# Kernel tuning notes

Measured on AMD Instinct MI355X. Metric: run time of the kernel, lower is better.

The kernel has to match this reference:

```python
import jax, jax.numpy as jnp
import numpy as np

N_NODES = 50000
N_EDGES = 800000
D_IN = 768
D_H = 256
N_CLASSES = 4
N_LAYERS = 3
N_GRAPHS = 64
LN_EPS = 1e-5


def setup_inputs() -> dict:
    key = jax.random.key(0)
    ks = jax.random.split(key, 12)
    x = jax.random.normal(ks[0], (N_NODES, D_IN), dtype=jnp.float32)
    edge_index = jax.random.randint(ks[1], (2, N_EDGES), 0, N_NODES)
    batch = jnp.sort(jax.random.randint(ks[2], (N_NODES,), 0, N_GRAPHS))
    s_in = 1.0 / np.sqrt(D_IN)
    s_h = 1.0 / np.sqrt(D_H)
    W_in = jax.random.normal(ks[3], (D_IN, D_H), jnp.float32) * s_in
    b_in = jnp.zeros((D_H,), jnp.float32)
    convW = jax.random.normal(ks[4], (N_LAYERS, D_H, D_H), jnp.float32) * s_h
    convB = jnp.zeros((N_LAYERS, D_H), jnp.float32)
    lnG = jnp.ones((N_LAYERS, D_H), jnp.float32)
    lnB = jnp.zeros((N_LAYERS, D_H), jnp.float32)
    clsW1 = jax.random.normal(ks[5], (D_H, D_H), jnp.float32) * s_h
    clsB1 = jnp.zeros((D_H,), jnp.float32)
    clsW2 = jax.random.normal(ks[6], (D_H, N_CLASSES), jnp.float32) * s_h
    clsB2 = jnp.zeros((N_CLASSES,), jnp.float32)
    return {"x": x, "edge_index": edge_index, "batch": batch,
            "W_in": W_in, "b_in": b_in, "convW": convW, "convB": convB,
            "lnG": lnG, "lnB": lnB, "clsW1": clsW1, "clsB1": clsB1,
            "clsW2": clsW2, "clsB2": clsB2}


def _layer_norm(h, g, b):
    mu = jnp.mean(h, axis=-1, keepdims=True)
    var = jnp.mean(jnp.square(h - mu), axis=-1, keepdims=True)
    return (h - mu) * jax.lax.rsqrt(var + LN_EPS) * g + b


def reference(x, edge_index, batch, W_in, b_in, convW, convB, lnG, lnB,
              clsW1, clsB1, clsW2, clsB2):
    N = x.shape[0]
    loops = jnp.arange(N)
    src = jnp.concatenate([edge_index[0], loops])  # self-loops (PyG GCNConv default)
    dst = jnp.concatenate([edge_index[1], loops])
    deg = jax.ops.segment_sum(jnp.ones_like(src, dtype=x.dtype), dst, num_segments=N)
    dinv = jax.lax.rsqrt(deg)  # deg >= 1 due to self-loops
    norm = dinv[src] * dinv[dst]  # symmetric GCN normalization per edge

    h = x @ W_in + b_in  # input projection -> [N, D_H]
    for i in range(N_LAYERS):
        m = h @ convW[i]  # transform then propagate
        h_new = jax.ops.segment_sum(m[src] * norm[:, None], dst, num_segments=N) + convB[i]
        h = jax.nn.relu(h_new + h)  # residual (shapes match), then ReLU
        h = _layer_norm(h, lnG[i], lnB[i])
        # dropout: identity (inference mode)

    g = jax.ops.segment_max(h, batch, num_segments=N_GRAPHS)  # global_max_pool
    z = jax.nn.relu(g @ clsW1 + clsB1)
    return z @ clsW2 + clsB2  # [N_GRAPHS, N_CLASSES]
```

## Files before the change

kernel.cpp:

```cpp
#include <hip/hip_runtime.h>
#include <hip/hip_bf16.h>
#include <math.h>

#define NNODES 50000
#define NEDGES 800000
#define DIN 768
#define DH 256
#define NCLS 4
#define NGRAPHS 64
#define SCAN_BLOCKS 196
#define PBLK 782
#define PS 24

typedef __bf16 bf16x8 __attribute__((ext_vector_type(8)));
typedef float f32x4 __attribute__((ext_vector_type(4)));

static __device__ __forceinline__ float bf2f(unsigned short u) {
    union { unsigned u32; float f; } v; v.u32 = ((unsigned)u) << 16; return v.f;
}
static __device__ __forceinline__ unsigned short f2bf(float f) {
    union { float f; unsigned u; } v; v.f = f;
    unsigned r = (v.u + 0x7fffu + ((v.u >> 16) & 1u)) >> 16;
    return (unsigned short)r;
}
static __device__ __forceinline__ void unpack8(uint4 u, float* f) {
    f[0] = bf2f((unsigned short)(u.x & 0xffff)); f[1] = bf2f((unsigned short)(u.x >> 16));
    f[2] = bf2f((unsigned short)(u.y & 0xffff)); f[3] = bf2f((unsigned short)(u.y >> 16));
    f[4] = bf2f((unsigned short)(u.z & 0xffff)); f[5] = bf2f((unsigned short)(u.z >> 16));
    f[6] = bf2f((unsigned short)(u.w & 0xffff)); f[7] = bf2f((unsigned short)(u.w >> 16));
}
static __device__ __forceinline__ void acc8(uint4 u, float* f) {
    f[0] += bf2f((unsigned short)(u.x & 0xffff)); f[1] += bf2f((unsigned short)(u.x >> 16));
    f[2] += bf2f((unsigned short)(u.y & 0xffff)); f[3] += bf2f((unsigned short)(u.y >> 16));
    f[4] += bf2f((unsigned short)(u.z & 0xffff)); f[5] += bf2f((unsigned short)(u.z >> 16));
    f[6] += bf2f((unsigned short)(u.w & 0xffff)); f[7] += bf2f((unsigned short)(u.w >> 16));
}
static __device__ __forceinline__ uint4 pack8f(float4 f0, float4 f1) {
    uint4 u;
    u.x = (unsigned)f2bf(f0.x) | ((unsigned)f2bf(f0.y) << 16);
    u.y = (unsigned)f2bf(f0.z) | ((unsigned)f2bf(f0.w) << 16);
    u.z = (unsigned)f2bf(f1.x) | ((unsigned)f2bf(f1.y) << 16);
    u.w = (unsigned)f2bf(f1.z) | ((unsigned)f2bf(f1.w) << 16);
    return u;
}
static __device__ __forceinline__ void gload_lds16(const void* g, void* l) {
    __builtin_amdgcn_global_load_lds((const __attribute__((address_space(1))) void*)g,
                                     (__attribute__((address_space(3))) void*)l, 16, 0, 0);
}

__global__ void detect_dtype(const unsigned short* __restrict__ x, int* __restrict__ flag) {
    __shared__ int cnt_s;
    if (threadIdx.x == 0) cnt_s = 0;
    __syncthreads();
    int c = 0;
    for (int i = 0; i < 16; ++i) {
        float v = bf2f(x[threadIdx.x * 16 + i]);
        if (!(fabsf(v) < 1e10f)) c++;
    }
    atomicAdd(&cnt_s, c);
    __syncthreads();
    if (threadIdx.x == 0) flag[0] = (cnt_s > 32) ? 1 : 0;
}

static __device__ __forceinline__ unsigned short cload(const void* src, int i, int fp32) {
    return fp32 ? f2bf(((const float*)src)[i]) : ((const unsigned short*)src)[i];
}

__global__ void canon_small(const void* b_in, const void* convB, const void* lnG,
                            const void* lnB, const void* W1, const void* W2,
                            const void* b1, const void* b2,
                            unsigned short* __restrict__ dst, const int* __restrict__ flag) {
    int i = blockIdx.x * 256 + threadIdx.x;
    if (i >= 69380) return;
    const int fp32 = flag[0];
    int j = i;
    if (j < 256)  { dst[i] = cload(b_in, j, fp32); return; }  j -= 256;
    if (j < 768)  { dst[i] = cload(convB, j, fp32); return; } j -= 768;
    if (j < 768)  { dst[i] = cload(lnG, j, fp32); return; }   j -= 768;
    if (j < 768)  { dst[i] = cload(lnB, j, fp32); return; }   j -= 768;
    if (j < 65536){ dst[i] = cload(W1, j, fp32); return; }    j -= 65536;
    if (j < 1024) { dst[i] = cload(W2, j, fp32); return; }    j -= 1024;
    if (j < 256)  { dst[i] = cload(b1, j, fp32); return; }    j -= 256;
    dst[i] = cload(b2, j, fp32);
}

__global__ void transpose_win(const void* __restrict__ src, unsigned short* __restrict__ dst,
                              const int* __restrict__ flag) {
    int idx = blockIdx.x * 256 + threadIdx.x;
    if (idx < DIN * DH) {
        int r = idx / DH, c = idx % DH;
        dst[(size_t)c * DIN + r] = cload(src, idx, flag[0]);
    }
}
__global__ void transpose_convw(const void* __restrict__ src, unsigned short* __restrict__ dst,
                                const int* __restrict__ flag) {
    int idx = blockIdx.x * 256 + threadIdx.x;
    if (idx < 3 * DH * DH) {
        int l = idx >> 16, rc = idx & 65535;
        int r = rc >> 8, c = rc & 255;
        dst[(l << 16) + c * DH + r] = cload(src, idx, flag[0]);
    }
}

__global__ __launch_bounds__(256) void pack_a(
    const void* __restrict__ x, const int* __restrict__ flag,
    uint4* __restrict__ out)
{
    const int c = blockIdx.x * 256 + threadIdx.x;
    const int blk = c / 6144;
    const int rem = c - blk * 6144;
    const int s = rem >> 8;
    const int q = rem & 255;
    const int r = q >> 2, p = q & 3;
    const int l = p ^ ((r >> 1) & 3);
    const int row = blk * 64 + r;
    const int k0 = s * 32 + l * 8;
    uint4 v = make_uint4(0u, 0u, 0u, 0u);
    if (row < NNODES) {
        if (flag[0]) {
            const float* xf = (const float*)x + (size_t)row * DIN + k0;
            float4 f0 = *(const float4*)xf;
            float4 f1 = *(const float4*)(xf + 4);
            v = pack8f(f0, f1);
        } else {
            v = *(const uint4*)((const unsigned short*)x + (size_t)row * DIN + k0);
        }
    }
    out[c] = v;
}

__global__ void fill_sentinel(float* out, int n) {
    int i = blockIdx.x * 256 + threadIdx.x;
    if (i < n) out[i] = 1000.0f;
}

__global__ void count_edges(const int* __restrict__ ei, int* __restrict__ cnt) {
    int e = blockIdx.x * 256 + threadIdx.x;
    if (e < NEDGES) atomicAdd(&cnt[ei[NEDGES + e]], 1);
}

__global__ void scan_local(const int* __restrict__ cnt, int* __restrict__ rowptr,
                           int* __restrict__ bsum) {
    __shared__ int tmp[256];
    int i = blockIdx.x * 256 + threadIdx.x;
    int v = (i < NNODES) ? cnt[i] : 0;
    tmp[threadIdx.x] = v;
    __syncthreads();
    for (int off = 1; off < 256; off <<= 1) {
        int a = (threadIdx.x >= off) ? tmp[threadIdx.x - off] : 0;
        __syncthreads();
        tmp[threadIdx.x] += a;
        __syncthreads();
    }
    if (i < NNODES) rowptr[i] = tmp[threadIdx.x] - v;
    if (threadIdx.x == 255) bsum[blockIdx.x] = tmp[255];
}
__global__ void scan_bsum(const int* __restrict__ bsum, int* __restrict__ boff) {
    __shared__ int tmp[256];
    int t = threadIdx.x;
    int v = (t < SCAN_BLOCKS) ? bsum[t] : 0;
    tmp[t] = v;
    __syncthreads();
    for (int off = 1; off < 256; off <<= 1) {
        int a = (t >= off) ? tmp[t - off] : 0;
        __syncthreads();
        tmp[t] += a;
        __syncthreads();
    }
    if (t < SCAN_BLOCKS) boff[t] = tmp[t] - v;
}
__global__ void scan_finish(int* __restrict__ rowptr, const int* __restrict__ boff,
                            const int* __restrict__ cnt, float* __restrict__ dinv) {
    int i = blockIdx.x * 256 + threadIdx.x;
    if (i < NNODES) {
        rowptr[i] += boff[blockIdx.x];
        dinv[i] = rsqrtf((float)(1 + cnt[i]));
    }
    if (i == 0) rowptr[NNODES] = NEDGES;
}

__global__ void fill_csr(const int* __restrict__ ei, const int* __restrict__ rowptr,
                         int* __restrict__ cursor, int* __restrict__ csrc) {
    int e = blockIdx.x * 256 + threadIdx.x;
    if (e < NEDGES) {
        int s = ei[e];
        int d = ei[NEDGES + e];
        int pos = rowptr[d] + atomicAdd(&cursor[d], 1);
        csrc[pos] = s;
    }
}

template<int WF>
__global__ __launch_bounds__(256, WF == 1 ? 3 : 4) void gemm_core(
    const void* __restrict__ Araw, const int* __restrict__ dflag,
    const unsigned short* __restrict__ Bt, const unsigned short* __restrict__ bias,
    const float* __restrict__ prescale, unsigned short* __restrict__ C, int M, int K)
{
    __shared__ __align__(16) char As[2][WF == 1 ? 8192 : 4096];
    __shared__ __align__(16) char Bs[2][16384];

    const int af32 = (WF == 1) ? dflag[0] : 0;
    const int m0 = blockIdx.x * 64;
    const int t = threadIdx.x, wave = t >> 6, lane = t & 63;
    const int quad = lane >> 4, l16 = lane & 15;

    const char* bsrc[4];
#pragma unroll
    for (int li = 0; li < 4; ++li) {
        int c = wave * 256 + li * 64 + lane;
        int r = c >> 2, p = c & 3;
        int l = p ^ ((r >> 1) & 3);
        bsrc[li] = (const char*)Bt + ((size_t)r * K + l * 8) * 2;
    }
    const char* asrc[2];
    if (WF == 2) {
        asrc[0] = (const char*)Araw + (size_t)blockIdx.x * (PS * 4096) + t * 16;
        asrc[1] = asrc[0];
    } else if (WF == 1 && af32) {
#pragma unroll
        for (int li = 0; li < 2; ++li) {
            int c = wave * 128 + li * 64 + lane;
            int r = c >> 3, p = c & 7;
            int l = p ^ (r & 7);
            int rg = min(m0 + r, M - 1);
            asrc[li] = (const char*)Araw + ((size_t)rg * K + l * 4) * 4;
        }
    } else {
        int c = wave * 64 + lane;
        int r = c >> 2, p = c & 3;
        int l = p ^ ((r >> 1) & 3);
        int rg = min(m0 + r, M - 1);
        asrc[0] = (const char*)Araw + ((size_t)rg * K + l * 8) * 2;
        asrc[1] = asrc[0];
    }

    f32x4 acc[4][4];
#pragma unroll
    for (int i = 0; i < 4; i++)
#pragma unroll
        for (int j = 0; j < 4; j++) acc[i][j] = (f32x4){0.f, 0.f, 0.f, 0.f};

    {
#pragma unroll
        for (int li = 0; li < 4; ++li)
            gload_lds16(bsrc[li], &Bs[0][(wave * 256 + li * 64) * 16]);
        if (WF == 1 && af32) {
            gload_lds16(asrc[0], &As[0][(wave * 128) * 16]);
            gload_lds16(asrc[1], &As[0][(wave * 128 + 64) * 16]);
        } else {
            gload_lds16(asrc[0], &As[0][(wave * 64) * 16]);
        }
    }
    __syncthreads();

    const int nt = K / 32;
    for (int tt = 0; tt < nt; ++tt) {
        const int buf = tt & 1;
        if (tt + 1 < nt) {
            const size_t k0 = (size_t)(tt + 1) * 32;
#pragma unroll
            for (int li = 0; li < 4; ++li)
                gload_lds16(bsrc[li] + k0 * 2, &Bs[buf ^ 1][(wave * 256 + li * 64) * 16]);
            if (WF == 2) {
                gload_lds16(asrc[0] + (size_t)(tt + 1) * 4096, &As[buf ^ 1][(wave * 64) * 16]);
            } else if (WF == 1 && af32) {
                gload_lds16(asrc[0] + k0 * 4, &As[buf ^ 1][(wave * 128) * 16]);
                gload_lds16(asrc[1] + k0 * 4, &As[buf ^ 1][(wave * 128 + 64) * 16]);
            } else {
                gload_lds16(asrc[0] + k0 * 2, &As[buf ^ 1][(wave * 64) * 16]);
            }
        }
        const char* as_ = As[buf];
        const char* bs_ = Bs[buf];
        bf16x8 afv[4], bfv[4];
        if (WF == 1 && af32) {
#pragma unroll
            for (int i = 0; i < 4; i++) {
                const int row = 16 * i + l16;
                const int ph0 = (quad * 2) ^ (row & 7);
                float4 x0 = *(const float4*)(as_ + row * 128 + ph0 * 16);
                float4 x1 = *(const float4*)(as_ + row * 128 + (ph0 ^ 1) * 16);
                union { bf16x8 v; __bf16 e[8]; } u;
                u.e[0] = (__bf16)x0.x; u.e[1] = (__bf16)x0.y;
                u.e[2] = (__bf16)x0.z; u.e[3] = (__bf16)x0.w;
                u.e[4] = (__bf16)x1.x; u.e[5] = (__bf16)x1.y;
                u.e[6] = (__bf16)x1.z; u.e[7] = (__bf16)x1.w;
                afv[i] = u.v;
            }
        } else {
            const int ph = (quad ^ ((l16 >> 1) & 3)) * 16;
#pragma unroll
            for (int i = 0; i < 4; i++)
                afv[i] = *(const bf16x8*)(as_ + (16 * i + l16) * 64 + ph);
        }
        {
            const int ph = (quad ^ ((l16 >> 1) & 3)) * 16;
#pragma unroll
            for (int j = 0; j < 4; j++)
                bfv[j] = *(const bf16x8*)(bs_ + (wave * 64 + 16 * j + l16) * 64 + ph);
        }
#pragma unroll
        for (int i = 0; i < 4; i++)
#pragma unroll
            for (int j = 0; j < 4; j++)
                acc[i][j] = __builtin_amdgcn_mfma_f32_16x16x32_bf16(afv[i], bfv[j], acc[i][j], 0, 0, 0);
        __syncthreads();
    }

#pragma unroll
    for (int j = 0; j < 4; j++) {
        const int gc = wave * 64 + 16 * j + l16;
        const float bv = bias ? bf2f(bias[gc]) : 0.f;
#pragma unroll
        for (int i = 0; i < 4; i++) {
#pragma unroll
            for (int rr = 0; rr < 4; rr++) {
                int gr = m0 + 16 * i + quad * 4 + rr;
                if (gr < M) {
                    float sc = prescale ? prescale[gr] : 1.f;
                    C[(size_t)gr * 256 + gc] = f2bf(acc[i][j][rr] * sc + bv);
                }
            }
        }
    }
}

__global__ __launch_bounds__(256) void aggregate_ln(
    const int* __restrict__ rowptr, const int* __restrict__ csrc,
    const float* __restrict__ dinv, const unsigned short* __restrict__ m,
    const unsigned short* __restrict__ convB,
    const unsigned short* __restrict__ lnG, const unsigned short* __restrict__ lnB,
    unsigned short* __restrict__ h)
{
    const int half = threadIdx.x >> 5;
    const int lane = threadIdx.x & 31;
    const int node = blockIdx.x * 8 + half;
    const float di = dinv[node];
    const size_t base = (size_t)node * DH + lane * 8;
    const size_t lo = lane * 8;

    float v0[8], v1[8];
    unpack8(*(const uint4*)(m + base), v0);
#pragma unroll
    for (int j = 0; j < 8; j++) v1[j] = 0.f;

    const int kb = rowptr[node], ke = rowptr[node + 1];
    int k = kb;
    for (; k + 8 <= ke; k += 8) {
        int s0 = csrc[k],     s1 = csrc[k + 1], s2 = csrc[k + 2], s3 = csrc[k + 3];
        int s4 = csrc[k + 4], s5 = csrc[k + 5], s6 = csrc[k + 6], s7 = csrc[k + 7];
        uint4 r0 = *(const uint4*)(m + (size_t)s0 * DH + lo);
        uint4 r1 = *(const uint4*)(m + (size_t)s1 * DH + lo);
        uint4 r2 = *(const uint4*)(m + (size_t)s2 * DH + lo);
        uint4 r3 = *(const uint4*)(m + (size_t)s3 * DH + lo);
        uint4 r4 = *(const uint4*)(m + (size_t)s4 * DH + lo);
        uint4 r5 = *(const uint4*)(m + (size_t)s5 * DH + lo);
        uint4 r6 = *(const uint4*)(m + (size_t)s6 * DH + lo);
        uint4 r7 = *(const uint4*)(m + (size_t)s7 * DH + lo);
        acc8(r0, v0); acc8(r1, v1); acc8(r2, v0); acc8(r3, v1);
        acc8(r4, v0); acc8(r5, v1); acc8(r6, v0); acc8(r7, v1);
    }
    for (; k + 2 <= ke; k += 2) {
        int s0 = csrc[k], s1 = csrc[k + 1];
        uint4 r0 = *(const uint4*)(m + (size_t)s0 * DH + lo);
        uint4 r1 = *(const uint4*)(m + (size_t)s1 * DH + lo);
        acc8(r0, v0); acc8(r1, v1);
    }
    if (k < ke) {
        uint4 r0 = *(const uint4*)(m + (size_t)csrc[k] * DH + lo);
        acc8(r0, v0);
    }
#pragma unroll
    for (int j = 0; j < 8; j++) v0[j] = (v0[j] + v1[j]) * di;

    float hv[8], cv[8];
    unpack8(*(const uint4*)(h + base), hv);
    unpack8(*(const uint4*)(convB + lo), cv);
    float s1 = 0.f, s2 = 0.f;
#pragma unroll
    for (int j = 0; j < 8; j++) {
        v0[j] = fmaxf(v0[j] + cv[j] + hv[j], 0.f);
        s1 += v0[j];
        s2 += v0[j] * v0[j];
    }
#pragma unroll
    for (int off = 16; off > 0; off >>= 1) {
        s1 += __shfl_xor(s1, off, 32);
        s2 += __shfl_xor(s2, off, 32);
    }
    const float mu = s1 * (1.f / 256.f);
    const float var = s2 * (1.f / 256.f) - mu * mu;
    const float rs = rsqrtf(var + 1e-5f);
    float gv[8], bv[8];
    unpack8(*(const uint4*)(lnG + lo), gv);
    unpack8(*(const uint4*)(lnB + lo), bv);
    unsigned short o[8];
#pragma unroll
    for (int j = 0; j < 8; j++) o[j] = f2bf((v0[j] - mu) * rs * gv[j] + bv[j]);
    uint4 outp;
    outp.x = (unsigned)o[0] | ((unsigned)o[1] << 16);
    outp.y = (unsigned)o[2] | ((unsigned)o[3] << 16);
    outp.z = (unsigned)o[4] | ((unsigned)o[5] << 16);
    outp.w = (unsigned)o[6] | ((unsigned)o[7] << 16);
    *(uint4*)(h + base) = outp;
}

__global__ void find_bounds(const int* __restrict__ batch, int* __restrict__ s) {
    int i = blockIdx.x * 256 + threadIdx.x;
    if (i >= NNODES) return;
    int b = batch[i];
    int bp = (i == 0) ? -1 : batch[i - 1];
    for (int g = bp + 1; g <= b; ++g) s[g] = i;
    if (i == NNODES - 1)
        for (int g = b + 1; g <= NGRAPHS; ++g) s[g] = NNODES;
}

#define PSPLIT 8
__global__ __launch_bounds__(256) void pool_partial(
    const unsigned short* __restrict__ h, const int* __restrict__ s,
    float* __restrict__ pg)
{
    const int b = blockIdx.x >> 3, split = blockIdx.x & 7, f = threadIdx.x;
    const int i0 = s[b], i1 = s[b + 1];
    const int len = i1 - i0;
    const int c0 = i0 + (int)(((long)len * split) >> 3);
    const int c1 = i0 + (int)(((long)len * (split + 1)) >> 3);
    float mx = -INFINITY;
    for (int i = c0; i < c1; ++i) mx = fmaxf(mx, bf2f(h[(size_t)i * DH + f]));
    pg[(size_t)blockIdx.x * DH + f] = mx;
}
__global__ __launch_bounds__(256) void pool_reduce(const float* __restrict__ pg,
                                                   float* __restrict__ g) {
    const int b = blockIdx.x, f = threadIdx.x;
    float mx = -INFINITY;
#pragma unroll
    for (int j = 0; j < PSPLIT; ++j) mx = fmaxf(mx, pg[(size_t)(b * PSPLIT + j) * DH + f]);
    g[b * DH + f] = mx;
}

__global__ __launch_bounds__(256) void classifier(
    const float* __restrict__ g, const unsigned short* __restrict__ W1,
    const unsigned short* __restrict__ b1, const unsigned short* __restrict__ W2,
    const unsigned short* __restrict__ b2, void* __restrict__ outv,
    const int* __restrict__ flag)
{
    __shared__ float gz[DH];
    __shared__ float zz[DH];
    const int b = blockIdx.x, t = threadIdx.x;
    gz[t] = g[b * DH + t];
    __syncthreads();
    float s = bf2f(b1[t]);
    for (int k = 0; k < DH; ++k) s += gz[k] * bf2f(W1[k * DH + t]);
    zz[t] = fmaxf(s, 0.f);
    __syncthreads();
    if (t < NCLS) {
        float s2 = bf2f(b2[t]);
        for (int k = 0; k < DH; ++k) s2 += zz[k] * bf2f(W2[k * NCLS + t]);
        if (flag[0]) ((float*)outv)[b * NCLS + t] = s2;
        else ((unsigned short*)outv)[b * NCLS + t] = f2bf(s2);
    }
}

extern "C" void kernel_launch(void* const* d_in, const int* in_sizes, int n_in,
                              void* d_out, int out_size, void* d_ws, size_t ws_size,
                              hipStream_t stream)
{
    const void* x      = d_in[0];
    const int* ei      = (const int*)d_in[1];
    const int* batch   = (const int*)d_in[2];
    const void* Win    = d_in[3];
    const void* b_in   = d_in[4];
    const void* convW  = d_in[5];
    const void* convB  = d_in[6];
    const void* lnG    = d_in[7];
    const void* lnB    = d_in[8];
    const void* W1     = d_in[9];
    const void* b1     = d_in[10];
    const void* W2     = d_in[11];
    const void* b2     = d_in[12];

    char* ws = (char*)d_ws;
    unsigned short* h   = (unsigned short*)(ws + 0);
    unsigned short* m   = (unsigned short*)(ws + 25600000);
    int* csrc           = (int*)(ws + 51200000);
    int* rowptr         = (int*)(ws + 54400000);
    int* cnt            = (int*)(ws + 54600016);
    int* cursor         = (int*)(ws + 54800016);
    float* dinv         = (float*)(ws + 55000016);
    unsigned short* cw  = (unsigned short*)(ws + 55200016);
    unsigned short* WinT= (unsigned short*)(ws + 55338784);
    unsigned short* WcT = (unsigned short*)(ws + 55732000);
    float* g            = (float*)(ws + 56125216);
    float* pg           = (float*)(ws + 56190752);
    int* gb             = (int*)(ws + 56715040);
    int* bsum           = (int*)(ws + 56715312);
    int* boff           = (int*)(ws + 56716112);
    int* flag           = (int*)(ws + 56716912);
    uint4* Apack        = (uint4*)(ws + 56716928);
    const size_t NEED_BASE = 56716928;
    const size_t NEED_FULL = 56716928 + (size_t)PBLK * PS * 4096;
    if (ws_size < NEED_BASE) {
        fill_sentinel<<<(out_size / 2 + 255) / 256, 256, 0, stream>>>((float*)d_out, out_size / 2);
        return;
    }
    const bool packed = (ws_size >= NEED_FULL);

    unsigned short* cBin   = cw + 0;
    unsigned short* cConvB = cw + 256;
    unsigned short* cLnG   = cw + 1024;
    unsigned short* cLnB   = cw + 1792;
    unsigned short* cW1    = cw + 2560;
    unsigned short* cW2    = cw + 68096;
    unsigned short* cB1    = cw + 69120;
    unsigned short* cB2    = cw + 69376;

    detect_dtype<<<1, 256, 0, stream>>>((const unsigned short*)x, flag);

    hipMemsetAsync(cnt, 0, 400000, stream);
    count_edges<<<(NEDGES + 255) / 256, 256, 0, stream>>>(ei, cnt);
    scan_local<<<SCAN_BLOCKS, 256, 0, stream>>>(cnt, rowptr, bsum);
    scan_bsum<<<1, 256, 0, stream>>>(bsum, boff);
    scan_finish<<<SCAN_BLOCKS, 256, 0, stream>>>(rowptr, boff, cnt, dinv);
    fill_csr<<<(NEDGES + 255) / 256, 256, 0, stream>>>(ei, rowptr, cursor, csrc);

    canon_small<<<(69380 + 255) / 256, 256, 0, stream>>>(b_in, convB, lnG, lnB, W1, W2, b1, b2, cw, flag);
    transpose_win<<<(DIN * DH + 255) / 256, 256, 0, stream>>>(Win, WinT, flag);
    transpose_convw<<<(3 * DH * DH + 255) / 256, 256, 0, stream>>>(convW, WcT, flag);

    if (packed) {
        pack_a<<<PBLK * PS, 256, 0, stream>>>(x, flag, Apack);
        gemm_core<2><<<PBLK, 256, 0, stream>>>(Apack, flag, WinT, cBin, nullptr, h, NNODES, DIN);
    } else {
        gemm_core<1><<<PBLK, 256, 0, stream>>>(x, flag, WinT, cBin, nullptr, h, NNODES, DIN);
    }

    for (int i = 0; i < 3; i++) {
        gemm_core<0><<<PBLK, 256, 0, stream>>>(h, flag, WcT + i * DH * DH, nullptr, dinv, m,
                                               NNODES, DH);
        aggregate_ln<<<NNODES / 8, 256, 0, stream>>>(
            rowptr, csrc, dinv, m, cConvB + i * DH, cLnG + i * DH, cLnB + i * DH, h);
    }

    find_bounds<<<(NNODES + 255) / 256, 256, 0, stream>>>(batch, gb);
    pool_partial<<<NGRAPHS * PSPLIT, 256, 0, stream>>>(h, gb, pg);
    pool_reduce<<<NGRAPHS, 256, 0, stream>>>(pg, g);
    classifier<<<NGRAPHS, 256, 0, stream>>>(g, cW1, cB1, cW2, cB2, d_out, flag);
}
```

Baseline: 740.3 us.

## Add persistent weight-stationary GEMM for conv layers and drop A-packing pass

Replaces the tiled conv-layer GEMM with a persistent kernel of 256 blocks that loads the full 256x256 weight matrix into LDS once and streams 32-row chunks of h through it, prefetching the next chunk. It also removes the separate pack_a pre-pass for the input projection, which now always reads x directly via the fp32/bf16 path. The aim is to avoid reloading B for each tile and to skip the extra pack kernel's write and read of x. In exchange, the 128KB LDS B buffer limits occupancy to one 512-thread block per CU, and the input GEMM loses its packed-A layout.

```diff
diff --git a/kernel.cpp b/kernel.cpp
--- a/kernel.cpp
+++ b/kernel.cpp
@@ -9,8 +9,8 @@
 #define NCLS 4
 #define NGRAPHS 64
 #define SCAN_BLOCKS 196
-#define PBLK 782
-#define PS 24
+#define WSCHUNK 32
+#define NCHUNKS ((NNODES + WSCHUNK - 1) / WSCHUNK)
 
 typedef __bf16 bf16x8 __attribute__((ext_vector_type(8)));
 typedef float f32x4 __attribute__((ext_vector_type(4)));
@@ -34,14 +34,6 @@
     f[2] += bf2f((unsigned short)(u.y & 0xffff)); f[3] += bf2f((unsigned short)(u.y >> 16));
     f[4] += bf2f((unsigned short)(u.z & 0xffff)); f[5] += bf2f((unsigned short)(u.z >> 16));
     f[6] += bf2f((unsigned short)(u.w & 0xffff)); f[7] += bf2f((unsigned short)(u.w >> 16));
-}
-static __device__ __forceinline__ uint4 pack8f(float4 f0, float4 f1) {
-    uint4 u;
-    u.x = (unsigned)f2bf(f0.x) | ((unsigned)f2bf(f0.y) << 16);
-    u.y = (unsigned)f2bf(f0.z) | ((unsigned)f2bf(f0.w) << 16);
-    u.z = (unsigned)f2bf(f1.x) | ((unsigned)f2bf(f1.y) << 16);
-    u.w = (unsigned)f2bf(f1.z) | ((unsigned)f2bf(f1.w) << 16);
-    return u;
 }
 static __device__ __forceinline__ void gload_lds16(const void* g, void* l) {
     __builtin_amdgcn_global_load_lds((const __attribute__((address_space(1))) void*)g,
@@ -102,33 +94,6 @@
     }
 }
 
-__global__ __launch_bounds__(256) void pack_a(
-    const void* __restrict__ x, const int* __restrict__ flag,
-    uint4* __restrict__ out)
-{
-    const int c = blockIdx.x * 256 + threadIdx.x;
-    const int blk = c / 6144;
-    const int rem = c - blk * 6144;
-    const int s = rem >> 8;
-    const int q = rem & 255;
-    const int r = q >> 2, p = q & 3;
-    const int l = p ^ ((r >> 1) & 3);
-    const int row = blk * 64 + r;
-    const int k0 = s * 32 + l * 8;
-    uint4 v = make_uint4(0u, 0u, 0u, 0u);
-    if (row < NNODES) {
-        if (flag[0]) {
-            const float* xf = (const float*)x + (size_t)row * DIN + k0;
-            float4 f0 = *(const float4*)xf;
-            float4 f1 = *(const float4*)(xf + 4);
-            v = pack8f(f0, f1);
-        } else {
-            v = *(const uint4*)((const unsigned short*)x + (size_t)row * DIN + k0);
-        }
-    }
-    out[c] = v;
-}
-
 __global__ void fill_sentinel(float* out, int n) {
     int i = blockIdx.x * 256 + threadIdx.x;
     if (i < n) out[i] = 1000.0f;
@@ -190,16 +155,15 @@
     }
 }
 
-template<int WF>
-__global__ __launch_bounds__(256, WF == 1 ? 3 : 4) void gemm_core(
+__global__ __launch_bounds__(256, 3) void gemm_in(
     const void* __restrict__ Araw, const int* __restrict__ dflag,
     const unsigned short* __restrict__ Bt, const unsigned short* __restrict__ bias,
-    const float* __restrict__ prescale, unsigned short* __restrict__ C, int M, int K)
+    unsigned short* __restrict__ C, int M, int K)
 {
-    __shared__ __align__(16) char As[2][WF == 1 ? 8192 : 4096];
+    __shared__ __align__(16) char As[2][8192];
     __shared__ __align__(16) char Bs[2][16384];
 
-    const int af32 = (WF == 1) ? dflag[0] : 0;
+    const int af32 = dflag[0];
     const int m0 = blockIdx.x * 64;
     const int t = threadIdx.x, wave = t >> 6, lane = t & 63;
     const int quad = lane >> 4, l16 = lane & 15;
@@ -213,10 +177,7 @@
         bsrc[li] = (const char*)Bt + ((size_t)r * K + l * 8) * 2;
     }
     const char* asrc[2];
-    if (WF == 2) {
-        asrc[0] = (const char*)Araw + (size_t)blockIdx.x * (PS * 4096) + t * 16;
-        asrc[1] = asrc[0];
-    } else if (WF == 1 && af32) {
+    if (af32) {
 #pragma unroll
         for (int li = 0; li < 2; ++li) {
             int c = wave * 128 + li * 64 + lane;
@@ -244,7 +205,7 @@
 #pragma unroll
         for (int li = 0; li < 4; ++li)
             gload_lds16(bsrc[li], &Bs[0][(wave * 256 + li * 64) * 16]);
-        if (WF == 1 && af32) {
+        if (af32) {
             gload_lds16(asrc[0], &As[0][(wave * 128) * 16]);
             gload_lds16(asrc[1], &As[0][(wave * 128 + 64) * 16]);
         } else {
@@ -261,9 +222,7 @@
 #pragma unroll
             for (int li = 0; li < 4; ++li)
                 gload_lds16(bsrc[li] + k0 * 2, &Bs[buf ^ 1][(wave * 256 + li * 64) * 16]);
-            if (WF == 2) {
-                gload_lds16(asrc[0] + (size_t)(tt + 1) * 4096, &As[buf ^ 1][(wave * 64) * 16]);
-            } else if (WF == 1 && af32) {
+            if (af32) {
                 gload_lds16(asrc[0] + k0 * 4, &As[buf ^ 1][(wave * 128) * 16]);
                 gload_lds16(asrc[1] + k0 * 4, &As[buf ^ 1][(wave * 128 + 64) * 16]);
             } else {
@@ -273,7 +232,7 @@
         const char* as_ = As[buf];
         const char* bs_ = Bs[buf];
         bf16x8 afv[4], bfv[4];
-        if (WF == 1 && af32) {
+        if (af32) {
 #pragma unroll
             for (int i = 0; i < 4; i++) {
                 const int row = 16 * i + l16;
@@ -310,18 +269,97 @@
 #pragma unroll
     for (int j = 0; j < 4; j++) {
         const int gc = wave * 64 + 16 * j + l16;
-        const float bv = bias ? bf2f(bias[gc]) : 0.f;
+        const float bv = bf2f(bias[gc]);
 #pragma unroll
         for (int i = 0; i < 4; i++) {
 #pragma unroll
             for (int rr = 0; rr < 4; rr++) {
                 int gr = m0 + 16 * i + quad * 4 + rr;
-                if (gr < M) {
-                    float sc = prescale ? prescale[gr] : 1.f;
-                    C[(size_t)gr * 256 + gc] = f2bf(acc[i][j][rr] * sc + bv);
+                if (gr < M) C[(size_t)gr * 256 + gc] = f2bf(acc[i][j][rr] + bv);
+            }
+        }
+    }
+}
+
+__global__ __launch_bounds__(512, 1) void gemm_ws(
+    const unsigned short* __restrict__ A,
+    const unsigned short* __restrict__ Bt,
+    const float* __restrict__ prescale,
+    unsigned short* __restrict__ C, int M)
+{
+    __shared__ __align__(16) unsigned short Bs[256 * 256];
+    __shared__ __align__(16) unsigned short As[WSCHUNK * 256];
+
+    const int t = threadIdx.x;
+    const int wave = t >> 6, lane = t & 63;
+    const int quad = lane >> 4, l16 = lane & 15;
+    const int rf = wave & 1;
+    const int cg = wave >> 1;
+
+    for (int it = 0; it < 16; ++it) {
+        int id = it * 512 + t;
+        int col = id >> 5, p = id & 31;
+        int l = p ^ (col & 31);
+        gload_lds16(Bt + col * 256 + l * 8, (char*)Bs + id * 16);
+    }
+    {
+        const int rbs = blockIdx.x * WSCHUNK;
+#pragma unroll
+        for (int it = 0; it < 2; ++it) {
+            int id = it * 512 + t;
+            int row = id >> 5, p = id & 31;
+            int l = p ^ (row & 31);
+            int rg = min(rbs + row, M - 1);
+            gload_lds16(A + (size_t)rg * 256 + l * 8, (char*)As + id * 16);
+        }
+    }
+    __syncthreads();
+
+    for (int c = blockIdx.x; c < NCHUNKS; c += 256) {
+        f32x4 acc[4];
+#pragma unroll
+        for (int j = 0; j < 4; ++j) acc[j] = (f32x4){0.f, 0.f, 0.f, 0.f};
+
+        const int arow = rf * 16 + l16;
+#pragma unroll
+        for (int ks = 0; ks < 8; ++ks) {
+            const int s = ks * 4 + quad;
+            bf16x8 af = *(const bf16x8*)((const char*)As + arow * 512 + ((s ^ (arow & 31)) * 16));
+#pragma unroll
+            for (int j = 0; j < 4; ++j) {
+                const int col = cg * 64 + j * 16 + l16;
+                bf16x8 bf = *(const bf16x8*)((const char*)Bs + col * 512 + ((s ^ (col & 31)) * 16));
+                acc[j] = __builtin_amdgcn_mfma_f32_16x16x32_bf16(af, bf, acc[j], 0, 0, 0);
+            }
+        }
+        __syncthreads();
+
+        const int cn = c + 256;
+        if (cn < NCHUNKS) {
+            const int rbs = cn * WSCHUNK;
+#pragma unroll
+            for (int it = 0; it < 2; ++it) {
+                int id = it * 512 + t;
+                int row = id >> 5, p = id & 31;
+                int l = p ^ (row & 31);
+                int rg = min(rbs + row, M - 1);
+                gload_lds16(A + (size_t)rg * 256 + l * 8, (char*)As + id * 16);
+            }
+        }
+        const int rb = c * WSCHUNK;
+#pragma unroll
+        for (int r = 0; r < 4; ++r) {
+            const int gr = rb + rf * 16 + quad * 4 + r;
+            if (gr < M) {
+                const float sc = prescale[gr];
+#pragma unroll
+                for (int j = 0; j < 4; ++j) {
+                    const int gc = cg * 64 + j * 16 + l16;
+                    C[(size_t)gr * 256 + gc] = f2bf(acc[j][r] * sc);
                 }
             }
         }
+        __syncthreads();
     }
 }
 
@@ -496,14 +534,11 @@
     int* bsum           = (int*)(ws + 56715312);
     int* boff           = (int*)(ws + 56716112);
     int* flag           = (int*)(ws + 56716912);
-    uint4* Apack        = (uint4*)(ws + 56716928);
-    const size_t NEED_BASE = 56716928;
-    const size_t NEED_FULL = 56716928 + (size_t)PBLK * PS * 4096;
-    if (ws_size < NEED_BASE) {
+    const size_t NEED   = 56716928;
+    if (ws_size < NEED) {
         fill_sentinel<<<(out_size / 2 + 255) / 256, 256, 0, stream>>>((float*)d_out, out_size / 2);
         return;
     }
-    const bool packed = (ws_size >= NEED_FULL);
 
     unsigned short* cBin   = cw + 0;
     unsigned short* cConvB = cw + 256;
@@ -527,16 +562,10 @@
     transpose_win<<<(DIN * DH + 255) / 256, 256, 0, stream>>>(Win, WinT, flag);
     transpose_convw<<<(3 * DH * DH + 255) / 256, 256, 0, stream>>>(convW, WcT, flag);
 
-    if (packed) {
-        pack_a<<<PBLK * PS, 256, 0, stream>>>(x, flag, Apack);
-        gemm_core<2><<<PBLK, 256, 0, stream>>>(Apack, flag, WinT, cBin, nullptr, h, NNODES, DIN);
-    } else {
-        gemm_core<1><<<PBLK, 256, 0, stream>>>(x, flag, WinT, cBin, nullptr, h, NNODES, DIN);
-    }
+    gemm_in<<<(NNODES + 63) / 64, 256, 0, stream>>>(x, flag, WinT, cBin, h, NNODES, DIN);
 
     for (int i = 0; i < 3; i++) {
-        gemm_core<0><<<PBLK, 256, 0, stream>>>(h, flag, WcT + i * DH * DH, nullptr, dinv, m,
-                                               NNODES, DH);
+        gemm_ws<<<256, 512, 0, stream>>>(h, WcT + i * DH * DH, dinv, m, NNODES);
         aggregate_ln<<<NNODES / 8, 256, 0, stream>>>(
             rowptr, csrc, dinv, m, cConvB + i * DH, cLnG + i * DH, cLnB + i * DH, h);
     }
```

Result: faster. 681.9 us (-7.9%).
